# Kernel optimization log

Hardware: AMD Instinct MI355X
Metric: run time of the kernel (lower is better)

Reference implementation:

```python
import jax, jax.numpy as jnp
import numpy as np

N = 10000
E = 320000

def leaky(x):
    return jnp.where(x >= 0, x, 0.01 * x)

def spmm(rows, cols, vals, dense):
    # sparse(N,N) @ dense(N,D) via gather + segment-sum
    return jax.ops.segment_sum(vals[:, None] * dense[cols], rows, num_segments=N)

def setup_inputs() -> dict:
    key = jax.random.key(0)
    ks = jax.random.split(key, 16)
    def xav(k, shp):
        std = float(np.sqrt(2.0 / (shp[0] + shp[1])))
        return jax.random.normal(k, shp, dtype=jnp.float32) * std
    return {
        "x": jax.random.normal(ks[0], (N, 512), dtype=jnp.float32),
        "adj_rows": jax.random.randint(ks[1], (E,), 0, N, dtype=jnp.int32),
        "adj_cols": jax.random.randint(ks[2], (E,), 0, N, dtype=jnp.int32),
        "adj_vals": jax.random.uniform(ks[3], (E,), dtype=jnp.float32),
        "W1": xav(ks[4], (512, 256)), "b1": jnp.zeros((256,), jnp.float32),
        "Wc1a": xav(ks[5], (256, 128)), "bc1a": jnp.zeros((128,), jnp.float32),
        "Wc1b": xav(ks[6], (128, 64)), "bc1b": jnp.zeros((64,), jnp.float32),
        "Wc2a": xav(ks[7], (64, 128)), "bc2a": jnp.zeros((128,), jnp.float32),
        "Wc2b": xav(ks[8], (128, 256)), "bc2b": jnp.zeros((256,), jnp.float32),
        "W6": xav(ks[9], (256, 512)), "b6": jnp.zeros((512,), jnp.float32),
    }

def reference(x, adj_rows, adj_cols, adj_vals, W1, b1, Wc1a, bc1a, Wc1b, bc1b,
              Wc2a, bc2a, Wc2b, bc2b, W6, b6):
    # encode (eval mode: dropout is identity)
    h = spmm(adj_rows, adj_cols, adj_vals, x @ W1) + b1   # gc1
    h = leaky(h)
    z = leaky(h @ Wc1a + bc1a) @ Wc1b + bc1b              # classifier1, [N,64]
    # inner-product decoder with identity activation -> dense NxN adjacency
    A = z @ z.T                                            # [N,N]
    # decode: classifier2 then gc6 applied with the DENSE reconstructed adj
    h2 = leaky(z @ Wc2a + bc2a) @ Wc2b + bc2b              # [N,256]
    h2 = leaky(h2)
    out = A @ (h2 @ W6) + b6                               # [N,512]
    return (out, z)
```

## Files before the change

kernel.cpp:

```cpp
#include <hip/hip_runtime.h>
#include <hip/hip_bf16.h>

#define NROWS 10000
#define KPAD  10240

typedef __attribute__((ext_vector_type(8))) short bf16x8;
typedef __attribute__((ext_vector_type(4))) float f32x4;

__device__ __forceinline__ float leaky_f(float x) { return x >= 0.f ? x : 0.01f * x; }

__device__ __forceinline__ unsigned short f2bf(float f) {
    union { float f; unsigned int u; } v; v.f = f;
    unsigned int r = v.u + 0x7fffu + ((v.u >> 16) & 1u);
    return (unsigned short)(r >> 16);
}
__device__ __forceinline__ float bf2f(unsigned short h) {
    union { unsigned int u; float f; } v; v.u = ((unsigned int)h) << 16;
    return v.f;
}

__global__ void conv_all(const float* __restrict__ x, const float* __restrict__ W1,
                         const float* __restrict__ Wc1a, const float* __restrict__ Wc1b,
                         const float* __restrict__ Wc2a, const float* __restrict__ Wc2b,
                         const float* __restrict__ W6,
                         unsigned short* __restrict__ XHI,
                         unsigned short* __restrict__ o1, unsigned short* __restrict__ o2,
                         unsigned short* __restrict__ o3, unsigned short* __restrict__ o4,
                         unsigned short* __restrict__ o5, unsigned short* __restrict__ o6,
                         int* __restrict__ counts, unsigned short* __restrict__ Zt,
                         unsigned short* __restrict__ H2t) {
    int gid = blockIdx.x * 256 + threadIdx.x;
    if (gid < 1280000) {
        float4 v = ((const float4*)x)[gid];
        ushort4 h;
        h.x = f2bf(v.x); h.y = f2bf(v.y); h.z = f2bf(v.z); h.w = f2bf(v.w);
        ((ushort4*)XHI)[gid] = h;
    } else if (gid < 1411072) {
        int i = gid - 1280000, k = i >> 8, n = i & 255;
        o1[n * 512 + k] = f2bf(W1[i]);
    } else if (gid < 1443840) {
        int i = gid - 1411072, k = i >> 7, n = i & 127;
        o2[n * 256 + k] = f2bf(Wc1a[i]);
    } else if (gid < 1452032) {
        int i = gid - 1443840, k = i >> 6, n = i & 63;
        o3[n * 128 + k] = f2bf(Wc1b[i]);
    } else if (gid < 1460224) {
        int i = gid - 1452032, k = i >> 7, n = i & 127;
        o4[n * 64 + k] = f2bf(Wc2a[i]);
    } else if (gid < 1492992) {
        int i = gid - 1460224, k = i >> 8, n = i & 255;
        o5[n * 128 + k] = f2bf(Wc2b[i]);
    } else if (gid < 1624064) {
        int i = gid - 1492992, k = i >> 9, n = i & 511;
        o6[n * 256 + k] = f2bf(W6[i]);
    } else if (gid < 1634064) {
        counts[gid - 1624064] = 0;
    } else if (gid < 1649424) {
        int i = gid - 1634064;
        Zt[(size_t)(i / 240) * KPAD + 10000 + (i % 240)] = 0;
    } else if (gid < 1710864) {
        int i = gid - 1649424;
        H2t[(size_t)(i / 240) * KPAD + 10000 + (i % 240)] = 0;
    }
}

__global__ void hist_kernel(const int* __restrict__ rows, int* __restrict__ counts, int E) {
    int i = blockIdx.x * blockDim.x + threadIdx.x;
    if (i < E) atomicAdd(&counts[rows[i]], 1);
}

__global__ __launch_bounds__(1024)
void scan_kernel(const int* __restrict__ counts, int* __restrict__ starts,
                 int* __restrict__ cursor, int n) {
    __shared__ int buf[1024];
    int tid = threadIdx.x;
    int base = tid * 10;
    int v[10];
    int local = 0;
#pragma unroll
    for (int j = 0; j < 10; ++j) {
        int i = base + j;
        v[j] = (i < n) ? counts[i] : 0;
        local += v[j];
    }
    buf[tid] = local;
    __syncthreads();
    for (int off = 1; off < 1024; off <<= 1) {
        int t = (tid >= off) ? buf[tid - off] : 0;
        __syncthreads();
        buf[tid] += t;
        __syncthreads();
    }
    int run = buf[tid] - local;
#pragma unroll
    for (int j = 0; j < 10; ++j) {
        int i = base + j;
        if (i < n) { starts[i] = run; cursor[i] = run; run += v[j]; }
    }
    if (tid == 1023) starts[n] = buf[1023];
}

__global__ void scatter_kernel(const int* __restrict__ rows, const int* __restrict__ cols,
                               const float* __restrict__ vals, int* __restrict__ cursor,
                               int* __restrict__ cols_s, float* __restrict__ vals_s, int E) {
    int i = blockIdx.x * blockDim.x + threadIdx.x;
    if (i < E) {
        int pos = atomicAdd(&cursor[rows[i]], 1);
        cols_s[pos] = cols[i];
        vals_s[pos] = vals[i];
    }
}

__global__ __launch_bounds__(64)
void spmm_leaky_kernel(const int* __restrict__ starts, const int* __restrict__ cols_s,
                       const float* __restrict__ vals_s, const unsigned short* __restrict__ C1b,
                       const float* __restrict__ b1, unsigned short* __restrict__ Hb) {
    int r = blockIdx.x;
    int t = threadIdx.x;
    float4 a0 = ((const float4*)b1)[t];
    float4 a1 = {0.f, 0.f, 0.f, 0.f};
    float4 a2 = {0.f, 0.f, 0.f, 0.f};
    float4 a3 = {0.f, 0.f, 0.f, 0.f};
    int s = starts[r], e = starts[r + 1];
    int p = s;
    for (; p + 4 <= e; p += 4) {
        int c0 = cols_s[p], c1 = cols_s[p + 1], c2 = cols_s[p + 2], c3 = cols_s[p + 3];
        float v0 = vals_s[p], v1 = vals_s[p + 1], v2 = vals_s[p + 2], v3 = vals_s[p + 3];
        ushort4 s0 = ((const ushort4*)(C1b + (size_t)c0 * 256))[t];
        ushort4 s1 = ((const ushort4*)(C1b + (size_t)c1 * 256))[t];
        ushort4 s2 = ((const ushort4*)(C1b + (size_t)c2 * 256))[t];
        ushort4 s3 = ((const ushort4*)(C1b + (size_t)c3 * 256))[t];
        a0.x += v0 * bf2f(s0.x); a0.y += v0 * bf2f(s0.y);
        a0.z += v0 * bf2f(s0.z); a0.w += v0 * bf2f(s0.w);
        a1.x += v1 * bf2f(s1.x); a1.y += v1 * bf2f(s1.y);
        a1.z += v1 * bf2f(s1.z); a1.w += v1 * bf2f(s1.w);
        a2.x += v2 * bf2f(s2.x); a2.y += v2 * bf2f(s2.y);
        a2.z += v2 * bf2f(s2.z); a2.w += v2 * bf2f(s2.w);
        a3.x += v3 * bf2f(s3.x); a3.y += v3 * bf2f(s3.y);
        a3.z += v3 * bf2f(s3.z); a3.w += v3 * bf2f(s3.w);
    }
    for (; p < e; ++p) {
        int c0 = cols_s[p];
        float v0 = vals_s[p];
        ushort4 s0 = ((const ushort4*)(C1b + (size_t)c0 * 256))[t];
        a0.x += v0 * bf2f(s0.x); a0.y += v0 * bf2f(s0.y);
        a0.z += v0 * bf2f(s0.z); a0.w += v0 * bf2f(s0.w);
    }
    ushort4 h;
    h.x = f2bf(leaky_f(a0.x + a1.x + a2.x + a3.x));
    h.y = f2bf(leaky_f(a0.y + a1.y + a2.y + a3.y));
    h.z = f2bf(leaky_f(a0.z + a1.z + a2.z + a3.z));
    h.w = f2bf(leaky_f(a0.w + a1.w + a2.w + a3.w));
    ((ushort4*)Hb)[(size_t)r * 64 + t] = h;
}

template<int ACT, int WF32, int WBF, int WTB>
__global__ __launch_bounds__(256)
void gemm_mfma(const unsigned short* __restrict__ A, const unsigned short* __restrict__ Bt,
               const float* __restrict__ bias, float* __restrict__ Cf,
               unsigned short* __restrict__ Cb, unsigned short* __restrict__ Ct,
               int ldt, int M, int N, int K) {
    __shared__ short sA[64][72];
    __shared__ short sB[64][72];
    const int bm = blockIdx.x * 64;
    const int bn = blockIdx.y * 64;
    const int tid = threadIdx.x;
    const int lane = tid & 63, wid = tid >> 6;
    const int wm = wid & 1, wn = wid >> 1;
    const int l15 = lane & 15, kg = lane >> 4;

    f32x4 acc[2][2];
#pragma unroll
    for (int i = 0; i < 2; i++)
#pragma unroll
        for (int j = 0; j < 2; j++) acc[i][j] = (f32x4){0.f, 0.f, 0.f, 0.f};

    for (int k0 = 0; k0 < K; k0 += 64) {
#pragma unroll
        for (int it = 0; it < 2; ++it) {
            int idx = tid + it * 256;
            int r = idx >> 3, s = idx & 7;
            int gm = bm + r;
            uint4 va = {0u, 0u, 0u, 0u};
            if (gm < M) va = *(const uint4*)(A + (size_t)gm * K + k0 + s * 8);
            *(uint4*)(&sA[r][s * 8]) = va;
            uint4 vb = *(const uint4*)(Bt + (size_t)(bn + r) * K + k0 + s * 8);
            *(uint4*)(&sB[r][s * 8]) = vb;
        }
        __syncthreads();
        bf16x8 a[2][2], b[2][2];
#pragma unroll
        for (int i = 0; i < 2; i++)
#pragma unroll
            for (int ks = 0; ks < 2; ++ks) {
                a[i][ks] = *(const bf16x8*)(&sA[wm * 32 + i * 16 + l15][kg * 8 + ks * 32]);
                b[i][ks] = *(const bf16x8*)(&sB[wn * 32 + i * 16 + l15][kg * 8 + ks * 32]);
            }
#pragma unroll
        for (int ks = 0; ks < 2; ++ks)
#pragma unroll
            for (int i = 0; i < 2; i++)
#pragma unroll
                for (int j = 0; j < 2; j++)
                    acc[i][j] = __builtin_amdgcn_mfma_f32_16x16x32_bf16(a[i][ks], b[j][ks], acc[i][j], 0, 0, 0);
        __syncthreads();
    }

#pragma unroll
    for (int i = 0; i < 2; i++) {
        int row0 = wm * 32 + i * 16 + kg * 4;
#pragma unroll
        for (int j = 0; j < 2; j++) {
            int col = bn + wn * 32 + j * 16 + l15;
            float bv = bias ? bias[col] : 0.f;
            ushort4 tw;
#pragma unroll
            for (int r = 0; r < 4; r++) {
                int grow = bm + row0 + r;
                float v = acc[i][j][r] + bv;
                if (ACT) v = leaky_f(v);
                if (WF32) { if (grow < M) Cf[(size_t)grow * N + col] = v; }
                if (WBF)  { if (grow < M) Cb[(size_t)grow * N + col] = f2bf(v); }
                if (WTB)  ((unsigned short*)&tw)[r] = f2bf(v);
            }
            if (WTB && (bm + row0) < M)
                *(ushort4*)(&Ct[(size_t)col * ldt + bm + row0]) = tw;
        }
    }
}

__global__ __launch_bounds__(256)
void fused_encdec(const unsigned short* __restrict__ H,
                  const unsigned short* __restrict__ Wa,
                  const unsigned short* __restrict__ Wb,
                  const unsigned short* __restrict__ Wc,
                  const unsigned short* __restrict__ Wd,
                  const float* __restrict__ ba, const float* __restrict__ bb,
                  const float* __restrict__ bc, const float* __restrict__ bd,
                  float* __restrict__ Zf, unsigned short* __restrict__ Zb,
                  unsigned short* __restrict__ Zt, unsigned short* __restrict__ H2t,
                  int M) {
    __shared__ short sA[64][72];
    __shared__ short sB[128][72];
    __shared__ short sT[64][136];
    __shared__ short sWb[64][136];
    __shared__ short sZ[64][72];
    __shared__ short sB2[256][72];
    const int bm = blockIdx.x * 64;
    const int tid = threadIdx.x;
    const int lane = tid & 63, wid = tid >> 6;
    const int wm = wid & 1, wn = wid >> 1;
    const int l15 = lane & 15, kg = lane >> 4;

#pragma unroll
    for (int it = 0; it < 4; ++it) {
        int idx = tid + it * 256;
        int r = idx >> 4, s = idx & 15;
        *(uint4*)(&sWb[r][s * 8]) = *(const uint4*)(Wb + r * 128 + s * 8);
    }

    f32x4 accA[2][4];
#pragma unroll
    for (int i = 0; i < 2; i++)
#pragma unroll
        for (int j = 0; j < 4; j++) accA[i][j] = (f32x4){0.f, 0.f, 0.f, 0.f};

    for (int k0 = 0; k0 < 256; k0 += 64) {
#pragma unroll
        for (int it = 0; it < 2; ++it) {
            int idx = tid + it * 256;
            int r = idx >> 3, s = idx & 7;
            int gm = bm + r;
            uint4 va = {0u, 0u, 0u, 0u};
            if (gm < M) va = *(const uint4*)(H + (size_t)gm * 256 + k0 + s * 8);
            *(uint4*)(&sA[r][s * 8]) = va;
        }
#pragma unroll
        for (int it = 0; it < 4; ++it) {
            int idx = tid + it * 256;
            int r = idx >> 3, s = idx & 7;
            *(uint4*)(&sB[r][s * 8]) = *(const uint4*)(Wa + r * 256 + k0 + s * 8);
        }
        __syncthreads();
#pragma unroll
        for (int ks = 0; ks < 2; ++ks) {
            bf16x8 a[2], b[4];
#pragma unroll
            for (int i = 0; i < 2; i++)
                a[i] = *(const bf16x8*)(&sA[wm * 32 + i * 16 + l15][kg * 8 + ks * 32]);
#pragma unroll
            for (int j = 0; j < 4; j++)
                b[j] = *(const bf16x8*)(&sB[wn * 64 + j * 16 + l15][kg * 8 + ks * 32]);
#pragma unroll
            for (int i = 0; i < 2; i++)
#pragma unroll
                for (int j = 0; j < 4; j++)
                    accA[i][j] = __builtin_amdgcn_mfma_f32_16x16x32_bf16(a[i], b[j], accA[i][j], 0, 0, 0);
        }
        __syncthreads();
    }
#pragma unroll
    for (int i = 0; i < 2; i++) {
        int row0 = wm * 32 + i * 16 + kg * 4;
#pragma unroll
        for (int j = 0; j < 4; j++) {
            int col = wn * 64 + j * 16 + l15;
            float bv = ba[col];
#pragma unroll
            for (int r = 0; r < 4; r++)
                sT[row0 + r][col] = f2bf(leaky_f(accA[i][j][r] + bv));
        }
    }
    __syncthreads();
#pragma unroll
    for (int it = 0; it < 4; ++it) {
        int idx = tid + it * 256;
        int r = idx >> 3, s = idx & 7;
        *(uint4*)(&sB[r][s * 8]) = *(const uint4*)(Wc + r * 64 + s * 8);
    }

    f32x4 accB[2][2];
#pragma unroll
    for (int i = 0; i < 2; i++)
#pragma unroll
        for (int j = 0; j < 2; j++) accB[i][j] = (f32x4){0.f, 0.f, 0.f, 0.f};
#pragma unroll
    for (int kc = 0; kc < 4; ++kc) {
        bf16x8 a[2], b[2];
#pragma unroll
        for (int i = 0; i < 2; i++)
            a[i] = *(const bf16x8*)(&sT[wm * 32 + i * 16 + l15][kc * 32 + kg * 8]);
#pragma unroll
        for (int j = 0; j < 2; j++)
            b[j] = *(const bf16x8*)(&sWb[wn * 32 + j * 16 + l15][kc * 32 + kg * 8]);
#pragma unroll
        for (int i = 0; i < 2; i++)
#pragma unroll
            for (int j = 0; j < 2; j++)
                accB[i][j] = __builtin_amdgcn_mfma_f32_16x16x32_bf16(a[i], b[j], accB[i][j], 0, 0, 0);
    }
#pragma unroll
    for (int i = 0; i < 2; i++) {
        int row0 = wm * 32 + i * 16 + kg * 4;
#pragma unroll
        for (int j = 0; j < 2; j++) {
            int col = wn * 32 + j * 16 + l15;
            float bv = bb[col];
            ushort4 tw;
#pragma unroll
            for (int r = 0; r < 4; r++) {
                int grow = bm + row0 + r;
                float v = accB[i][j][r] + bv;
                unsigned short zb = f2bf(v);
                if (grow < M) {
                    Zf[(size_t)grow * 64 + col] = v;
                    Zb[(size_t)grow * 64 + col] = zb;
                }
                sZ[row0 + r][col] = (short)zb;
                ((unsigned short*)&tw)[r] = zb;
            }
            if ((bm + row0) < M)
                *(ushort4*)(&Zt[(size_t)col * KPAD + bm + row0]) = tw;
        }
    }
    __syncthreads();

    f32x4 accC[2][4];
#pragma unroll
    for (int i = 0; i < 2; i++)
#pragma unroll
        for (int j = 0; j < 4; j++) accC[i][j] = (f32x4){0.f, 0.f, 0.f, 0.f};
#pragma unroll
    for (int ks = 0; ks < 2; ++ks) {
        bf16x8 a[2], b[4];
#pragma unroll
        for (int i = 0; i < 2; i++)
            a[i] = *(const bf16x8*)(&sZ[wm * 32 + i * 16 + l15][kg * 8 + ks * 32]);
#pragma unroll
        for (int j = 0; j < 4; j++)
            b[j] = *(const bf16x8*)(&sB[wn * 64 + j * 16 + l15][kg * 8 + ks * 32]);
#pragma unroll
        for (int i = 0; i < 2; i++)
#pragma unroll
            for (int j = 0; j < 4; j++)
                accC[i][j] = __builtin_amdgcn_mfma_f32_16x16x32_bf16(a[i], b[j], accC[i][j], 0, 0, 0);
    }
    __syncthreads();
#pragma unroll
    for (int i = 0; i < 2; i++) {
        int row0 = wm * 32 + i * 16 + kg * 4;
#pragma unroll
        for (int j = 0; j < 4; j++) {
            int col = wn * 64 + j * 16 + l15;
            float bv = bc[col];
#pragma unroll
            for (int r = 0; r < 4; r++)
                sT[row0 + r][col] = f2bf(leaky_f(accC[i][j][r] + bv));
        }
    }
    __syncthreads();

    f32x4 accD[2][8];
#pragma unroll
    for (int i = 0; i < 2; i++)
#pragma unroll
        for (int j = 0; j < 8; j++) accD[i][j] = (f32x4){0.f, 0.f, 0.f, 0.f};
    for (int k0 = 0; k0 < 128; k0 += 64) {
#pragma unroll
        for (int it = 0; it < 8; ++it) {
            int idx = tid + it * 256;
            int r = idx >> 3, s = idx & 7;
            *(uint4*)(&sB2[r][s * 8]) = *(const uint4*)(Wd + r * 128 + k0 + s * 8);
        }
        __syncthreads();
#pragma unroll
        for (int ks = 0; ks < 2; ++ks) {
            bf16x8 a[2], b[8];
#pragma unroll
            for (int i = 0; i < 2; i++)
                a[i] = *(const bf16x8*)(&sT[wm * 32 + i * 16 + l15][k0 + ks * 32 + kg * 8]);
#pragma unroll
            for (int j = 0; j < 8; j++)
                b[j] = *(const bf16x8*)(&sB2[wn * 128 + j * 16 + l15][kg * 8 + ks * 32]);
#pragma unroll
            for (int i = 0; i < 2; i++)
#pragma unroll
                for (int j = 0; j < 8; j++)
                    accD[i][j] = __builtin_amdgcn_mfma_f32_16x16x32_bf16(a[i], b[j], accD[i][j], 0, 0, 0);
        }
        __syncthreads();
    }
#pragma unroll
    for (int i = 0; i < 2; i++) {
        int row0 = wm * 32 + i * 16 + kg * 4;
#pragma unroll
        for (int j = 0; j < 8; j++) {
            int col = wn * 128 + j * 16 + l15;
            float bv = bd[col];
            ushort4 tw;
#pragma unroll
            for (int r = 0; r < 4; r++)
                ((unsigned short*)&tw)[r] = f2bf(leaky_f(accD[i][j][r] + bv));
            if ((bm + row0) < M)
                *(ushort4*)(&H2t[(size_t)col * KPAD + bm + row0]) = tw;
        }
    }
}

__global__ __launch_bounds__(256)
void sgemm_sk(const unsigned short* __restrict__ Zt, const unsigned short* __restrict__ H2t,
              float* __restrict__ part) {
    __shared__ short sA[64][72];
    __shared__ short sB[64][72];
    const int bn = blockIdx.x * 64;
    const int kc = blockIdx.y;
    const int tid = threadIdx.x;
    const int lane = tid & 63, wid = tid >> 6;
    const int wm = wid & 1, wn = wid >> 1;
    const int l15 = lane & 15, kg = lane >> 4;

    f32x4 acc[2][2];
#pragma unroll
    for (int i = 0; i < 2; i++)
#pragma unroll
        for (int j = 0; j < 2; j++) acc[i][j] = (f32x4){0.f, 0.f, 0.f, 0.f};

    for (int kk = 0; kk < 4; ++kk) {
        int k0 = kc * 256 + kk * 64;
#pragma unroll
        for (int it = 0; it < 2; ++it) {
            int idx = tid + it * 256;
            int r = idx >> 3, s = idx & 7;
            *(uint4*)(&sA[r][s * 8]) = *(const uint4*)(Zt + (size_t)r * KPAD + k0 + s * 8);
            *(uint4*)(&sB[r][s * 8]) = *(const uint4*)(H2t + (size_t)(bn + r) * KPAD + k0 + s * 8);
        }
        __syncthreads();
        bf16x8 a[2][2], b[2][2];
#pragma unroll
        for (int i = 0; i < 2; i++)
#pragma unroll
            for (int ks = 0; ks < 2; ++ks) {
                a[i][ks] = *(const bf16x8*)(&sA[wm * 32 + i * 16 + l15][kg * 8 + ks * 32]);
                b[i][ks] = *(const bf16x8*)(&sB[wn * 32 + i * 16 + l15][kg * 8 + ks * 32]);
            }
#pragma unroll
        for (int ks = 0; ks < 2; ++ks)
#pragma unroll
            for (int i = 0; i < 2; i++)
#pragma unroll
                for (int j = 0; j < 2; j++)
                    acc[i][j] = __builtin_amdgcn_mfma_f32_16x16x32_bf16(a[i][ks], b[j][ks], acc[i][j], 0, 0, 0);
        __syncthreads();
    }
#pragma unroll
    for (int i = 0; i < 2; i++) {
        int row0 = wm * 32 + i * 16 + kg * 4;
#pragma unroll
        for (int j = 0; j < 2; j++) {
            int col = bn + wn * 32 + j * 16 + l15;
#pragma unroll
            for (int r = 0; r < 4; r++)
                part[((size_t)kc * 64 + row0 + r) * 256 + col] = acc[i][j][r];
        }
    }
}

__global__ void reduce_S2(const float* __restrict__ part, unsigned short* __restrict__ S2b) {
    int i = blockIdx.x * blockDim.x + threadIdx.x;
    if (i < 64 * 256) {
        float s = 0.f;
#pragma unroll
        for (int c = 0; c < 40; ++c) s += part[(size_t)c * (64 * 256) + i];
        S2b[i] = f2bf(s);
    }
}

extern "C" void kernel_launch(void* const* d_in, const int* in_sizes, int n_in,
                              void* d_out, int out_size, void* d_ws, size_t ws_size,
                              hipStream_t stream) {
    const float* x    = (const float*)d_in[0];
    const int*   rows = (const int*)d_in[1];
    const int*   cols = (const int*)d_in[2];
    const float* vals = (const float*)d_in[3];
    const float* W1   = (const float*)d_in[4];
    const float* b1   = (const float*)d_in[5];
    const float* Wc1a = (const float*)d_in[6];
    const float* bc1a = (const float*)d_in[7];
    const float* Wc1b = (const float*)d_in[8];
    const float* bc1b = (const float*)d_in[9];
    const float* Wc2a = (const float*)d_in[10];
    const float* bc2a = (const float*)d_in[11];
    const float* Wc2b = (const float*)d_in[12];
    const float* bc2b = (const float*)d_in[13];
    const float* W6   = (const float*)d_in[14];
    const float* b6   = (const float*)d_in[15];

    const int N = NROWS;
    const int E = in_sizes[1];

    float* ws = (float*)d_ws;
    unsigned short* XHI  = (unsigned short*)(ws + 0);
    unsigned short* C1b  = (unsigned short*)(ws + 2560000);
    unsigned short* HHI  = (unsigned short*)(ws + 3840000);
    unsigned short* ZHI  = (unsigned short*)(ws + 5120000);
    unsigned short* ZT   = (unsigned short*)(ws + 5440000);
    unsigned short* H2T  = (unsigned short*)(ws + 5767680);
    float*          PART = ws + 7078400;
    unsigned short* S2B  = (unsigned short*)(ws + 7733760);
    unsigned short* W6ST = (unsigned short*)(ws + 7741952);
    unsigned short* W1T   = (unsigned short*)(ws + 7758336);
    unsigned short* WC1AT = (unsigned short*)(ws + 7823872);
    unsigned short* WC1BT = (unsigned short*)(ws + 7840256);
    unsigned short* WC2AT = (unsigned short*)(ws + 7844352);
    unsigned short* WC2BT = (unsigned short*)(ws + 7848448);
    unsigned short* W6T   = (unsigned short*)(ws + 7864832);

    int*   counts = (int*)(ws + 7930368);
    int*   starts = counts + 10000;
    int*   cursor = starts + 10001;
    int*   cols_s = cursor + 10000;
    float* vals_s = (float*)(cols_s + 320000);

    float* Out = (float*)d_out;
    float* Zp  = (float*)d_out + 5120000;

    const int GX = (N + 63) / 64;

    conv_all<<<6683, 256, 0, stream>>>(x, W1, Wc1a, Wc1b, Wc2a, Wc2b, W6, XHI,
                                       W1T, WC1AT, WC1BT, WC2AT, WC2BT, W6T,
                                       counts, ZT, H2T);

    hist_kernel<<<(E + 255) / 256, 256, 0, stream>>>(rows, counts, E);
    scan_kernel<<<1, 1024, 0, stream>>>(counts, starts, cursor, N);
    scatter_kernel<<<(E + 255) / 256, 256, 0, stream>>>(rows, cols, vals, cursor, cols_s, vals_s, E);

    gemm_mfma<0,0,1,0><<<dim3(GX, 4), 256, 0, stream>>>(XHI, W1T, nullptr,
                                                        nullptr, C1b, nullptr, 0, N, 256, 512);

    spmm_leaky_kernel<<<N, 64, 0, stream>>>(starts, cols_s, vals_s, C1b, b1, HHI);

    fused_encdec<<<GX, 256, 0, stream>>>(HHI, WC1AT, WC1BT, WC2AT, WC2BT,
                                         bc1a, bc1b, bc2a, bc2b,
                                         Zp, ZHI, ZT, H2T, N);

    sgemm_sk<<<dim3(4, 40), 256, 0, stream>>>(ZT, H2T, PART);
    reduce_S2<<<64, 256, 0, stream>>>(PART, S2B);

    gemm_mfma<0,0,0,1><<<dim3(1, 8), 256, 0, stream>>>(S2B, W6T, nullptr,
                                                       nullptr, nullptr, W6ST, 64, 64, 512, 256);

    gemm_mfma<0,1,0,0><<<dim3(GX, 8), 256, 0, stream>>>(ZHI, W6ST, b6,
                                                        Out, nullptr, nullptr, 0, N, 512, 64);
}
```

Measured before the change: 133.6 us.

## Halve fused encoder tile rows and fuse split-K reduce with W6 projection

The fused encoder/decoder kernel now processes 32 rows per block instead of 64, doubling the grid to about 313 blocks so more compute units are busy, while each wave does half the MFMA work. The split-K partial reduction and the small S2·W6 GEMM are merged into one kernel, s2_tail. This removes a launch and the S2 round trip through global memory. In exchange, each of the 8 s2_tail blocks redundantly re-reduces all 40 partial slices, and the smaller encoder tiles reload the shared weight matrices into LDS twice as often overall.

```diff
diff --git a/kernel.cpp b/kernel.cpp
--- a/kernel.cpp
+++ b/kernel.cpp
@@ -230,23 +230,23 @@
 }
 
 __global__ __launch_bounds__(256)
-void fused_encdec(const unsigned short* __restrict__ H,
-                  const unsigned short* __restrict__ Wa,
-                  const unsigned short* __restrict__ Wb,
-                  const unsigned short* __restrict__ Wc,
-                  const unsigned short* __restrict__ Wd,
-                  const float* __restrict__ ba, const float* __restrict__ bb,
-                  const float* __restrict__ bc, const float* __restrict__ bd,
-                  float* __restrict__ Zf, unsigned short* __restrict__ Zb,
-                  unsigned short* __restrict__ Zt, unsigned short* __restrict__ H2t,
-                  int M) {
-    __shared__ short sA[64][72];
+void fused_encdec32(const unsigned short* __restrict__ H,
+                    const unsigned short* __restrict__ Wa,
+                    const unsigned short* __restrict__ Wb,
+                    const unsigned short* __restrict__ Wc,
+                    const unsigned short* __restrict__ Wd,
+                    const float* __restrict__ ba, const float* __restrict__ bb,
+                    const float* __restrict__ bc, const float* __restrict__ bd,
+                    float* __restrict__ Zf, unsigned short* __restrict__ Zb,
+                    unsigned short* __restrict__ Zt, unsigned short* __restrict__ H2t,
+                    int M) {
+    __shared__ short sA[32][72];
     __shared__ short sB[128][72];
-    __shared__ short sT[64][136];
+    __shared__ short sT[32][136];
     __shared__ short sWb[64][136];
-    __shared__ short sZ[64][72];
+    __shared__ short sZ[32][72];
     __shared__ short sB2[256][72];
-    const int bm = blockIdx.x * 64;
+    const int bm = blockIdx.x * 32;
     const int tid = threadIdx.x;
     const int lane = tid & 63, wid = tid >> 6;
     const int wm = wid & 1, wn = wid >> 1;
@@ -259,17 +259,13 @@
         *(uint4*)(&sWb[r][s * 8]) = *(const uint4*)(Wb + r * 128 + s * 8);
     }
 
-    f32x4 accA[2][4];
-#pragma unroll
-    for (int i = 0; i < 2; i++)
-#pragma unroll
-        for (int j = 0; j < 4; j++) accA[i][j] = (f32x4){0.f, 0.f, 0.f, 0.f};
+    f32x4 accA[4];
+#pragma unroll
+    for (int j = 0; j < 4; j++) accA[j] = (f32x4){0.f, 0.f, 0.f, 0.f};
 
     for (int k0 = 0; k0 < 256; k0 += 64) {
-#pragma unroll
-        for (int it = 0; it < 2; ++it) {
-            int idx = tid + it * 256;
-            int r = idx >> 3, s = idx & 7;
+        {
+            int r = tid >> 3, s = tid & 7;
             int gm = bm + r;
             uint4 va = {0u, 0u, 0u, 0u};
             if (gm < M) va = *(const uint4*)(H + (size_t)gm * 256 + k0 + s * 8);
@@ -284,31 +280,26 @@
         __syncthreads();
 #pragma unroll
         for (int ks = 0; ks < 2; ++ks) {
-            bf16x8 a[2], b[4];
-#pragma unroll
-            for (int i = 0; i < 2; i++)
-                a[i] = *(const bf16x8*)(&sA[wm * 32 + i * 16 + l15][kg * 8 + ks * 32]);
+            bf16x8 a, b[4];
+            a = *(const bf16x8*)(&sA[wm * 16 + l15][kg * 8 + ks * 32]);
 #pragma unroll
             for (int j = 0; j < 4; j++)
                 b[j] = *(const bf16x8*)(&sB[wn * 64 + j * 16 + l15][kg * 8 + ks * 32]);
 #pragma unroll
-            for (int i = 0; i < 2; i++)
-#pragma unroll
-                for (int j = 0; j < 4; j++)
-                    accA[i][j] = __builtin_amdgcn_mfma_f32_16x16x32_bf16(a[i], b[j], accA[i][j], 0, 0, 0);
-        }
-        __syncthreads();
-    }
-#pragma unroll
-    for (int i = 0; i < 2; i++) {
-        int row0 = wm * 32 + i * 16 + kg * 4;
+            for (int j = 0; j < 4; j++)
+                accA[j] = __builtin_amdgcn_mfma_f32_16x16x32_bf16(a, b[j], accA[j], 0, 0, 0);
+        }
+        __syncthreads();
+    }
+    {
+        int row0 = wm * 16 + kg * 4;
 #pragma unroll
         for (int j = 0; j < 4; j++) {
             int col = wn * 64 + j * 16 + l15;
             float bv = ba[col];
 #pragma unroll
             for (int r = 0; r < 4; r++)
-                sT[row0 + r][col] = f2bf(leaky_f(accA[i][j][r] + bv));
+                sT[row0 + r][col] = f2bf(leaky_f(accA[j][r] + bv));
         }
     }
     __syncthreads();
@@ -319,29 +310,22 @@
         *(uint4*)(&sB[r][s * 8]) = *(const uint4*)(Wc + r * 64 + s * 8);
     }
 
-    f32x4 accB[2][2];
-#pragma unroll
-    for (int i = 0; i < 2; i++)
-#pragma unroll
-        for (int j = 0; j < 2; j++) accB[i][j] = (f32x4){0.f, 0.f, 0.f, 0.f};
+    f32x4 accB[2];
+#pragma unroll
+    for (int j = 0; j < 2; j++) accB[j] = (f32x4){0.f, 0.f, 0.f, 0.f};
 #pragma unroll
     for (int kc = 0; kc < 4; ++kc) {
-        bf16x8 a[2], b[2];
-#pragma unroll
-        for (int i = 0; i < 2; i++)
-            a[i] = *(const bf16x8*)(&sT[wm * 32 + i * 16 + l15][kc * 32 + kg * 8]);
+        bf16x8 a, b[2];
+        a = *(const bf16x8*)(&sT[wm * 16 + l15][kc * 32 + kg * 8]);
 #pragma unroll
         for (int j = 0; j < 2; j++)
             b[j] = *(const bf16x8*)(&sWb[wn * 32 + j * 16 + l15][kc * 32 + kg * 8]);
 #pragma unroll
-        for (int i = 0; i < 2; i++)
-#pragma unroll
-            for (int j = 0; j < 2; j++)
-                accB[i][j] = __builtin_amdgcn_mfma_f32_16x16x32_bf16(a[i], b[j], accB[i][j], 0, 0, 0);
-    }
-#pragma unroll
-    for (int i = 0; i < 2; i++) {
-        int row0 = wm * 32 + i * 16 + kg * 4;
+        for (int j = 0; j < 2; j++)
+            accB[j] = __builtin_amdgcn_mfma_f32_16x16x32_bf16(a, b[j], accB[j], 0, 0, 0);
+    }
+    {
+        int row0 = wm * 16 + kg * 4;
 #pragma unroll
         for (int j = 0; j < 2; j++) {
             int col = wn * 32 + j * 16 + l15;
@@ -350,7 +334,7 @@
 #pragma unroll
             for (int r = 0; r < 4; r++) {
                 int grow = bm + row0 + r;
-                float v = accB[i][j][r] + bv;
+                float v = accB[j][r] + bv;
                 unsigned short zb = f2bf(v);
                 if (grow < M) {
                     Zf[(size_t)grow * 64 + col] = v;
@@ -365,46 +349,37 @@
     }
     __syncthreads();
 
-    f32x4 accC[2][4];
-#pragma unroll
-    for (int i = 0; i < 2; i++)
-#pragma unroll
-        for (int j = 0; j < 4; j++) accC[i][j] = (f32x4){0.f, 0.f, 0.f, 0.f};
+    f32x4 accC[4];
+#pragma unroll
+    for (int j = 0; j < 4; j++) accC[j] = (f32x4){0.f, 0.f, 0.f, 0.f};
 #pragma unroll
     for (int ks = 0; ks < 2; ++ks) {
-        bf16x8 a[2], b[4];
-#pragma unroll
-        for (int i = 0; i < 2; i++)
-            a[i] = *(const bf16x8*)(&sZ[wm * 32 + i * 16 + l15][kg * 8 + ks * 32]);
+        bf16x8 a, b[4];
+        a = *(const bf16x8*)(&sZ[wm * 16 + l15][kg * 8 + ks * 32]);
 #pragma unroll
         for (int j = 0; j < 4; j++)
             b[j] = *(const bf16x8*)(&sB[wn * 64 + j * 16 + l15][kg * 8 + ks * 32]);
 #pragma unroll
-        for (int i = 0; i < 2; i++)
-#pragma unroll
-            for (int j = 0; j < 4; j++)
-                accC[i][j] = __builtin_amdgcn_mfma_f32_16x16x32_bf16(a[i], b[j], accC[i][j], 0, 0, 0);
+        for (int j = 0; j < 4; j++)
+            accC[j] = __builtin_amdgcn_mfma_f32_16x16x32_bf16(a, b[j], accC[j], 0, 0, 0);
     }
     __syncthreads();
-#pragma unroll
-    for (int i = 0; i < 2; i++) {
-        int row0 = wm * 32 + i * 16 + kg * 4;
+    {
+        int row0 = wm * 16 + kg * 4;
 #pragma unroll
         for (int j = 0; j < 4; j++) {
             int col = wn * 64 + j * 16 + l15;
             float bv = bc[col];
 #pragma unroll
             for (int r = 0; r < 4; r++)
-                sT[row0 + r][col] = f2bf(leaky_f(accC[i][j][r] + bv));
+                sT[row0 + r][col] = f2bf(leaky_f(accC[j][r] + bv));
         }
     }
     __syncthreads();
 
-    f32x4 accD[2][8];
-#pragma unroll
-    for (int i = 0; i < 2; i++)
-#pragma unroll
-        for (int j = 0; j < 8; j++) accD[i][j] = (f32x4){0.f, 0.f, 0.f, 0.f};
+    f32x4 accD[8];
+#pragma unroll
+    for (int j = 0; j < 8; j++) accD[j] = (f32x4){0.f, 0.f, 0.f, 0.f};
     for (int k0 = 0; k0 < 128; k0 += 64) {
 #pragma unroll
         for (int it = 0; it < 8; ++it) {
@@ -415,24 +390,19 @@
         __syncthreads();
 #pragma unroll
         for (int ks = 0; ks < 2; ++ks) {
-            bf16x8 a[2], b[8];
-#pragma unroll
-            for (int i = 0; i < 2; i++)
-                a[i] = *(const bf16x8*)(&sT[wm * 32 + i * 16 + l15][k0 + ks * 32 + kg * 8]);
+            bf16x8 a, b[8];
+            a = *(const bf16x8*)(&sT[wm * 16 + l15][k0 + ks * 32 + kg * 8]);
 #pragma unroll
             for (int j = 0; j < 8; j++)
                 b[j] = *(const bf16x8*)(&sB2[wn * 128 + j * 16 + l15][kg * 8 + ks * 32]);
 #pragma unroll
-            for (int i = 0; i < 2; i++)
-#pragma unroll
-                for (int j = 0; j < 8; j++)
-                    accD[i][j] = __builtin_amdgcn_mfma_f32_16x16x32_bf16(a[i], b[j], accD[i][j], 0, 0, 0);
-        }
-        __syncthreads();
-    }
-#pragma unroll
-    for (int i = 0; i < 2; i++) {
-        int row0 = wm * 32 + i * 16 + kg * 4;
+            for (int j = 0; j < 8; j++)
+                accD[j] = __builtin_amdgcn_mfma_f32_16x16x32_bf16(a, b[j], accD[j], 0, 0, 0);
+        }
+        __syncthreads();
+    }
+    {
+        int row0 = wm * 16 + kg * 4;
 #pragma unroll
         for (int j = 0; j < 8; j++) {
             int col = wn * 128 + j * 16 + l15;
@@ -440,7 +410,7 @@
             ushort4 tw;
 #pragma unroll
             for (int r = 0; r < 4; r++)
-                ((unsigned short*)&tw)[r] = f2bf(leaky_f(accD[i][j][r] + bv));
+                ((unsigned short*)&tw)[r] = f2bf(leaky_f(accD[j][r] + bv));
             if ((bm + row0) < M)
                 *(ushort4*)(&H2t[(size_t)col * KPAD + bm + row0]) = tw;
         }
@@ -505,13 +475,68 @@
     }
 }
 
-__global__ void reduce_S2(const float* __restrict__ part, unsigned short* __restrict__ S2b) {
-    int i = blockIdx.x * blockDim.x + threadIdx.x;
-    if (i < 64 * 256) {
+__global__ __launch_bounds__(256)
+void s2_tail(const float* __restrict__ part, const unsigned short* __restrict__ W6T,
+             unsigned short* __restrict__ W6ST) {
+    __shared__ short sS[64][264];
+    __shared__ short sB[64][72];
+    const int bn = blockIdx.x * 64;
+    const int tid = threadIdx.x;
+    const int lane = tid & 63, wid = tid >> 6;
+    const int wm = wid & 1, wn = wid >> 1;
+    const int l15 = lane & 15, kg = lane >> 4;
+
+    for (int idx = tid; idx < 64 * 256; idx += 256) {
         float s = 0.f;
 #pragma unroll
-        for (int c = 0; c < 40; ++c) s += part[(size_t)c * (64 * 256) + i];
-        S2b[i] = f2bf(s);
+        for (int c = 0; c < 40; ++c) s += part[(size_t)c * (64 * 256) + idx];
+        sS[idx >> 8][idx & 255] = (short)f2bf(s);
+    }
+    __syncthreads();
+
+    f32x4 acc[2][2];
+#pragma unroll
+    for (int i = 0; i < 2; i++)
+#pragma unroll
+        for (int j = 0; j < 2; j++) acc[i][j] = (f32x4){0.f, 0.f, 0.f, 0.f};
+
+    for (int k0 = 0; k0 < 256; k0 += 64) {
+#pragma unroll
+        for (int it = 0; it < 2; ++it) {
+            int idx = tid + it * 256;
+            int r = idx >> 3, s = idx & 7;
+            *(uint4*)(&sB[r][s * 8]) = *(const uint4*)(W6T + (size_t)(bn + r) * 256 + k0 + s * 8);
+        }
+        __syncthreads();
+        bf16x8 a[2][2], b[2][2];
+#pragma unroll
+        for (int i = 0; i < 2; i++)
+#pragma unroll
+            for (int ks = 0; ks < 2; ++ks) {
+                a[i][ks] = *(const bf16x8*)(&sS[wm * 32 + i * 16 + l15][k0 + kg * 8 + ks * 32]);
+                b[i][ks] = *(const bf16x8*)(&sB[wn * 32 + i * 16 + l15][kg * 8 + ks * 32]);
+            }
+#pragma unroll
+        for (int ks = 0; ks < 2; ++ks)
+#pragma unroll
+            for (int i = 0; i < 2; i++)
+#pragma unroll
+                for (int j = 0; j < 2; j++)
+                    acc[i][j] = __builtin_amdgcn_mfma_f32_16x16x32_bf16(a[i][ks], b[j][ks], acc[i][j], 0, 0, 0);
+        __syncthreads();
+    }
+#pragma unroll
+    for (int i = 0; i < 2; i++) {
+        int row0 = wm * 32 + i * 16 + kg * 4;
+#pragma unroll
+        for (int j = 0; j < 2; j++) {
+            int col = bn + wn * 32 + j * 16 + l15;
+            ushort4 tw;
+#pragma unroll
+            for (int r = 0; r < 4; r++)
+                ((unsigned short*)&tw)[r] = f2bf(acc[i][j][r]);
+            *(ushort4*)(&W6ST[(size_t)col * 64 + row0]) = tw;
+        }
     }
 }
 
@@ -546,7 +571,6 @@
     unsigned short* ZT   = (unsigned short*)(ws + 5440000);
     unsigned short* H2T  = (unsigned short*)(ws + 5767680);
     float*          PART = ws + 7078400;
-    unsigned short* S2B  = (unsigned short*)(ws + 7733760);
     unsigned short* W6ST = (unsigned short*)(ws + 7741952);
     unsigned short* W1T   = (unsigned short*)(ws + 7758336);
     unsigned short* WC1AT = (unsigned short*)(ws + 7823872);
@@ -565,6 +589,7 @@
     float* Zp  = (float*)d_out + 5120000;
 
     const int GX = (N + 63) / 64;
+    const int GX32 = (N + 31) / 32;
 
     conv_all<<<6683, 256, 0, stream>>>(x, W1, Wc1a, Wc1b, Wc2a, Wc2b, W6, XHI,
                                        W1T, WC1AT, WC1BT, WC2AT, WC2BT, W6T,
@@ -579,15 +604,13 @@
 
     spmm_leaky_kernel<<<N, 64, 0, stream>>>(starts, cols_s, vals_s, C1b, b1, HHI);
 
-    fused_encdec<<<GX, 256, 0, stream>>>(HHI, WC1AT, WC1BT, WC2AT, WC2BT,
-                                         bc1a, bc1b, bc2a, bc2b,
-                                         Zp, ZHI, ZT, H2T, N);
+    fused_encdec32<<<GX32, 256, 0, stream>>>(HHI, WC1AT, WC1BT, WC2AT, WC2BT,
+                                             bc1a, bc1b, bc2a, bc2b,
+                                             Zp, ZHI, ZT, H2T, N);
 
     sgemm_sk<<<dim3(4, 40), 256, 0, stream>>>(ZT, H2T, PART);
-    reduce_S2<<<64, 256, 0, stream>>>(PART, S2B);
-
-    gemm_mfma<0,0,0,1><<<dim3(1, 8), 256, 0, stream>>>(S2B, W6T, nullptr,
-                                                       nullptr, nullptr, W6ST, 64, 64, 512, 256);
+
+    s2_tail<<<8, 256, 0, stream>>>(PART, W6T, W6ST);
 
     gemm_mfma<0,1,0,0><<<dim3(GX, 8), 256, 0, stream>>>(ZHI, W6ST, b6,
                                                         Out, nullptr, nullptr, 0, N, 512, 64);
```

New measurement: 178.2 us. 1.33x slower.
